# Performance work log

Measured on AMD Instinct MI355X. Metric: run time of the kernel, lower is better.

The kernel has to match this reference:

```python
import math
import jax, jax.numpy as jnp
import numpy as np

NUM_BUCKETS = 32
MAX_DISTANCE = 128
N_HEADS = 16
D_KV = 64


def relative_position_bucket(rel_pos, num_buckets=NUM_BUCKETS, max_distance=MAX_DISTANCE):
    # bidirectional=True path of the original
    n = -rel_pos
    nb = num_buckets // 2
    ret = (n < 0).astype(jnp.int32) * nb
    n = jnp.abs(n)
    max_exact = nb // 2
    is_small = n < max_exact
    val_large = max_exact + (
        jnp.log(n.astype(jnp.float32) / max_exact)
        / math.log(max_distance / max_exact)
        * (nb - max_exact)
    ).astype(jnp.int32)
    val_large = jnp.minimum(val_large, nb - 1)
    return jnp.where(is_small, n, val_large) + ret


def setup_inputs() -> dict:
    key = jax.random.key(0)
    ks = jax.random.split(key, 6)
    B, S, D = 2, 2048, 1024
    inner = N_HEADS * D_KV  # 1024
    sc = 1.0 / math.sqrt(D)
    return {
        "x": jax.random.normal(ks[0], (B, S, D), dtype=jnp.float32),
        "Wq": jax.random.normal(ks[1], (D, inner), dtype=jnp.float32) * sc,
        "Wk": jax.random.normal(ks[2], (D, inner), dtype=jnp.float32) * sc,
        "Wv": jax.random.normal(ks[3], (D, inner), dtype=jnp.float32) * sc,
        "Wo": jax.random.normal(ks[4], (inner, D), dtype=jnp.float32) * sc,
        "rel_table": jax.random.normal(ks[5], (NUM_BUCKETS, N_HEADS), dtype=jnp.float32),
        "attention_mask": jnp.zeros((B, 1, 1, S), dtype=jnp.float32),
    }


def reference(x, Wq, Wk, Wv, Wo, rel_table, attention_mask):
    B, S, D = x.shape
    H, Dk = N_HEADS, D_KV

    q = (x @ Wq).reshape(B, S, H, Dk).transpose(0, 2, 1, 3)  # bhqd
    k = (x @ Wk).reshape(B, S, H, Dk).transpose(0, 2, 1, 3)
    v = (x @ Wv).reshape(B, S, H, Dk).transpose(0, 2, 1, 3)

    # NOTE: T5 attention has no 1/sqrt(d) scaling
    scores = jnp.einsum('bhqd,bhkd->bhqk', q.astype(jnp.float32), k.astype(jnp.float32))

    pos = jnp.arange(S)
    rel_pos = pos[None, :] - pos[:, None]  # [S,S] = k_pos - q_pos
    buckets = relative_position_bucket(rel_pos)
    position_bias = jnp.transpose(rel_table[buckets], (2, 0, 1))  # [H,S,S]

    scores = scores + position_bias[None, ...] + attention_mask
    weights = jax.nn.softmax(scores, axis=-1)
    out = jnp.einsum('bhqk,bhkd->bhqd', weights, v.astype(jnp.float32))
    out = out.transpose(0, 2, 1, 3).reshape(B, S, H * Dk).astype(x.dtype)
    out = out @ Wo
    return (out, position_bias)
```

## Files before the change

kernel.cpp:

```cpp
#include <hip/hip_runtime.h>
#include <hip/hip_bf16.h>
#include <math.h>
#include <stdint.h>

typedef __bf16 bf16_t;
typedef __attribute__((ext_vector_type(8))) __bf16 bf16x8;
typedef __attribute__((ext_vector_type(4))) float f32x4;
typedef float f32x4a __attribute__((ext_vector_type(4), aligned(4)));
typedef unsigned short u16;
typedef unsigned int u32;

#define DEV static __device__ __forceinline__
#define LOG2E 1.4426950408889634f

DEV u16 f2b(float f){ bf16_t h = (bf16_t)f; return __builtin_bit_cast(u16, h); }
DEV float b2f(u16 u){ bf16_t h = __builtin_bit_cast(bf16_t, u); return (float)h; }
DEV f32x4 mfma16(bf16x8 a, bf16x8 b, f32x4 c){
  return __builtin_amdgcn_mfma_f32_16x16x32_bf16(a, b, c, 0, 0, 0);
}

#if __has_builtin(__builtin_amdgcn_exp2f)
DEV float fexp2(float x){ return __builtin_amdgcn_exp2f(x); }
#else
DEV float fexp2(float x){ return exp2f(x); }
#endif

DEV void gld16(const void* g, void* l){
  __builtin_amdgcn_global_load_lds((const __attribute__((address_space(1))) u32*)g,
                                   (__attribute__((address_space(3))) u32*)l, 16, 0, 0);
}

DEV bf16x8 ldsA64(const u16* arr, int row, int ch){
  return *(const bf16x8*)&arr[row*64 + ((ch ^ (row&7))*8)];
}
DEV bf16x8 ldsA32(const u16* arr, int row, int ch){
  return *(const bf16x8*)&arr[row*32 + ((ch ^ ((row>>1)&3))*8)];
}

__global__ __launch_bounds__(256) void k_prep(const float* __restrict__ x,
                                              const float* __restrict__ Wq, const float* __restrict__ Wk,
                                              const float* __restrict__ Wv, const float* __restrict__ Wo,
                                              const float* __restrict__ rel_table, const float* __restrict__ mask,
                                              u16* __restrict__ xh, u16* __restrict__ xl,
                                              u16* __restrict__ wth, u16* __restrict__ wot,
                                              float* __restrict__ bt, float* __restrict__ bt2,
                                              float* __restrict__ msk2){
  __shared__ float tile[64][65];
  int bid = blockIdx.x;
  int t = threadIdx.x;
  if(bid < 4096){
    size_t i = ((size_t)bid*256 + t)*4;
    float4 v = *(const float4*)(x + i);
    ushort4 hv, lv; float f, hf;
    f=v.x; hv.x=f2b(f); hf=b2f(hv.x); lv.x=f2b(f-hf);
    f=v.y; hv.y=f2b(f); hf=b2f(hv.y); lv.y=f2b(f-hf);
    f=v.z; hv.z=f2b(f); hf=b2f(hv.z); lv.z=f2b(f-hf);
    f=v.w; hv.w=f2b(f); hf=b2f(hv.w); lv.w=f2b(f-hf);
    *(ushort4*)(xh+i) = hv;
    *(ushort4*)(xl+i) = lv;
  } else if(bid < 5120){
    int rr = bid - 4096;
    int z = rr >> 8, ky = (rr >> 4) & 15, nx = rr & 15;
    const float* W = (z==0)?Wq:((z==1)?Wk:((z==2)?Wv:Wo));
    int n0 = nx*64, k0 = ky*64;
    int r = t>>6, c = t&63;
    #pragma unroll
    for(int i=0;i<16;i++){
      int row = i*4 + r;
      tile[row][c] = W[(size_t)(k0+row)*1024 + n0 + c];
    }
    __syncthreads();
    #pragma unroll
    for(int i=0;i<16;i++){
      int nrow = i*4 + r;
      float v = tile[c][nrow];
      size_t o = (size_t)(n0+nrow)*1024 + k0 + c;
      if(z<3) wth[(size_t)z*1048576 + o] = f2b(v);
      else    wot[o] = f2b(v);
    }
  } else {
    int gid = (bid-5120)*256 + t;
    if(gid < 4096) msk2[gid] = mask[gid]*LOG2E;
    int h = gid >> 12, idx = gid & 4095;
    float v = 0.f;
    if(idx < 4095){
      int delta = idx - 2047;
      int n = -delta;
      int ret = 0;
      if(n < 0){ ret = 16; n = -n; }
      int bucket;
      if(n < 8) bucket = n + ret;
      else {
        float a = (float)log((double)n * 0.125);
        float rr2 = (float)((double)a / (double)2.7725887298583984f);
        int vl = 8 + (int)(rr2 * 8.0f);
        vl = vl > 15 ? 15 : vl;
        bucket = vl + ret;
      }
      v = rel_table[bucket*16 + h];
    }
    bt[gid] = v;
    bt2[gid] = v*LOG2E - 32.0f;
  }
}

__global__ __launch_bounds__(256) void k_gemm_qkv(const u16* __restrict__ xh, const u16* __restrict__ xl,
                                                  const u16* __restrict__ wth,
                                                  u16* __restrict__ qh, u16* __restrict__ ql,
                                                  u16* __restrict__ kh, u16* __restrict__ vt){
  __shared__ __align__(16) u16 SM[17408];
  u16* Ah = SM; u16* Al = SM+4096; u16* Bh = SM+8192;
  int z = blockIdx.z;
  const u16* WH = wth + (size_t)z*1048576;
  int m0 = blockIdx.y*128, n0 = blockIdx.x*128;
  int t = threadIdx.x, w = t>>6, lane = t&63, l16 = lane&15, g = lane>>4;
  f32x4 acc[4][4];
  #pragma unroll
  for(int i=0;i<4;i++)
    #pragma unroll
    for(int j=0;j<4;j++) acc[i][j] = {0.f,0.f,0.f,0.f};
  int rbase = (w>>1)*64, cbase = (w&1)*64;
  for(int k0=0;k0<1024;k0+=32){
    __syncthreads();
    #pragma unroll
    for(int jj=0;jj<6;jj++){
      int q = w + 4*jj;
      int arr = q>>3, sub = q&7;
      if(z!=0 && arr==1) continue;
      int row = sub*16 + (lane>>2);
      int lch = (lane&3) ^ ((row>>1)&3);
      const u16* src;
      if(arr==0)      src = xh + (size_t)(m0+row)*1024 + k0 + lch*8;
      else if(arr==1) src = xl + (size_t)(m0+row)*1024 + k0 + lch*8;
      else            src = WH + (size_t)(n0+row)*1024 + k0 + lch*8;
      gld16(src, &SM[q*512]);
    }
    __syncthreads();
    if(z!=0){
      bf16x8 ah[4];
      #pragma unroll
      for(int i=0;i<4;i++) ah[i] = ldsA32(Ah, rbase + i*16 + l16, g);
      #pragma unroll
      for(int j=0;j<4;j++){
        bf16x8 bh = ldsA32(Bh, cbase + j*16 + l16, g);
        #pragma unroll
        for(int i=0;i<4;i++)
          acc[i][j] = mfma16(ah[i], bh, acc[i][j]);
      }
    } else {
      bf16x8 ah[4], am[4];
      #pragma unroll
      for(int i=0;i<4;i++){
        int row = rbase + i*16 + l16;
        ah[i] = ldsA32(Ah, row, g);
        am[i] = ldsA32(Al, row, g);
      }
      #pragma unroll
      for(int j=0;j<4;j++){
        bf16x8 bh = ldsA32(Bh, cbase + j*16 + l16, g);
        #pragma unroll
        for(int i=0;i<4;i++){
          acc[i][j] = mfma16(ah[i], bh, acc[i][j]);
          acc[i][j] = mfma16(am[i], bh, acc[i][j]);
        }
      }
    }
  }
  if(z==2){
    __syncthreads();
    #pragma unroll
    for(int i=0;i<4;i++)
      #pragma unroll
      for(int j=0;j<4;j++)
        #pragma unroll
        for(int r=0;r<4;r++){
          int ml = rbase + i*16 + g*4 + r;
          int nl = cbase + j*16 + l16;
          SM[nl*136 + ml] = f2b(acc[i][j][r]);
        }
    __syncthreads();
    int bb = m0 >> 11;
    #pragma unroll
    for(int kk=0;kk<8;kk++){
      int id = t + 256*kk;
      int row = id>>4, ch = id&15;
      uint4 v = *(const uint4*)&SM[row*136 + ch*8];
      int n = n0 + row;
      size_t dst = ((size_t)(bb*16 + (n>>6))*64 + (n&63))*2048 + (m0&2047) + ch*8;
      *(uint4*)&vt[dst] = v;
    }
  } else {
    #pragma unroll
    for(int i=0;i<4;i++)
      #pragma unroll
      for(int j=0;j<4;j++)
        #pragma unroll
        for(int r=0;r<4;r++){
          int m = m0 + rbase + i*16 + g*4 + r;
          int n = n0 + cbase + j*16 + l16;
          float v = acc[i][j][r];
          if(z==0) v *= LOG2E;
          int b = m >> 11, s = m & 2047;
          int hh = n >> 6, d = n & 63;
          size_t a = ((size_t)(b*16+hh)*2048 + s)*64 + d;
          u16 hb = f2b(v);
          if(z==0){ qh[a]=hb; ql[a]=f2b(v - b2f(hb)); }
          else    { kh[a]=hb; }
        }
  }
}

__global__ __launch_bounds__(256) void k_attn(const u16* __restrict__ qh, const u16* __restrict__ ql,
                                              const u16* __restrict__ kh,
                                              const u16* __restrict__ vt, const float* __restrict__ bt2,
                                              const float* __restrict__ msk2,
                                              const float* __restrict__ bt, float* __restrict__ bias_out,
                                              u16* __restrict__ ao){
  __shared__ __align__(16) u16 SM[12800];
  u16* KH = SM; u16* VT = SM+4096;
  int bh = blockIdx.y, b = bh>>4, h = bh&15;
  int q0 = blockIdx.x*64;
  int t = threadIdx.x, w = t>>6, lane = t&63, l16 = lane&15, g = lane>>4;
  size_t base  = (size_t)bh*2048*64;
  size_t vbase = (size_t)bh*64*2048;
  u16* PSw = SM + 8192 + w*1152;
  const float* bt2h = bt2 + h*4096;
  const float* msk2b = msk2 + b*2048;
  size_t wbase = ((size_t)(bh*32 + blockIdx.x))*65536 + t*8;

  bf16x8 qfh[2], qfl[2];
  {
    int qr = q0 + w*16 + l16;
    size_t a0 = base + (size_t)qr*64 + g*8;
    qfh[0] = *(const bf16x8*)&qh[a0];
    qfl[0] = *(const bf16x8*)&ql[a0];
    qfh[1] = *(const bf16x8*)&qh[a0+32];
    qfl[1] = *(const bf16x8*)&ql[a0+32];
  }
  f32x4 O[4];
  float rs[4];
  #pragma unroll
  for(int jd=0;jd<4;jd++) O[jd] = {0.f,0.f,0.f,0.f};
  #pragma unroll
  for(int r=0;r<4;r++) rs[r] = 0.f;
  int qgbase = q0 + w*16 + g*4;

  for(int k0=0;k0<2048;k0+=64){
    __syncthreads();
    #pragma unroll
    for(int jj=0;jj<4;jj++){
      int q = w + 4*jj;
      int arr = q>>3, sub = q&7;
      int row = sub*8 + (lane>>3);
      int lch = (lane&7) ^ (row&7);
      const u16* src;
      if(arr==0) src = kh + base + (size_t)(k0+row)*64 + lch*8;
      else       src = vt + vbase + (size_t)row*2048 + k0 + lch*8;
      gld16(src, &SM[q*512]);
    }
    {
      size_t f = wbase + (size_t)(k0>>6)*2048;
      int hh = (int)(f >> 22);
      int rem = (int)(f & 4194303);
      int qq = rem >> 11;
      int kk = rem & 2047;
      const float* row = bt + hh*4096 + (kk - qq + 2047);
      f32x4a v0 = *(const f32x4a*)(row);
      f32x4a v1 = *(const f32x4a*)(row + 4);
      *(f32x4a*)(bias_out + f)     = v0;
      *(f32x4a*)(bias_out + f + 4) = v1;
    }
    f32x4 sc[4];
    {
      const float* bb = bt2h + (k0 + l16 + 2047 - qgbase);
      #pragma unroll
      for(int j=0;j<4;j++){
        f32x4a ld = *(const f32x4a*)(bb + j*16 - 3);
        float mk = msk2b[k0 + j*16 + l16];
        sc[j] = (f32x4){ld[3]+mk, ld[2]+mk, ld[1]+mk, ld[0]+mk};
      }
    }
    __syncthreads();
    #pragma unroll
    for(int j=0;j<4;j++){
      int krow = j*16 + l16;
      bf16x8 kfh0 = ldsA64(KH, krow, g);
      bf16x8 kfh1 = ldsA64(KH, krow, 4+g);
      f32x4 s = sc[j];
      s = mfma16(qfh[0], kfh0, s);
      s = mfma16(qfl[0], kfh0, s);
      s = mfma16(qfh[1], kfh1, s);
      s = mfma16(qfl[1], kfh1, s);
      sc[j] = s;
    }
    #pragma unroll
    for(int j=0;j<4;j++){
      #pragma unroll
      for(int r=0;r<4;r++){
        float p = fexp2(sc[j][r]);
        rs[r] += p;
        PSw[(g*4+r)*72 + j*16 + l16] = f2b(p);
      }
    }
    #pragma unroll
    for(int ds=0; ds<2; ds++){
      bf16x8 pa = *(const bf16x8*)&PSw[l16*72 + ds*32 + g*8];
      #pragma unroll
      for(int jd=0;jd<4;jd++){
        bf16x8 vb = ldsA64(VT, jd*16 + l16, ds*4 + g);
        O[jd] = mfma16(pa, vb, O[jd]);
      }
    }
  }
  #pragma unroll
  for(int r=0;r<4;r++){
    float v = rs[r];
    v += __shfl_xor(v,1,64);
    v += __shfl_xor(v,2,64);
    v += __shfl_xor(v,4,64);
    v += __shfl_xor(v,8,64);
    float inv = 1.f/v;
    int q = qgbase + r;
    size_t a = ((size_t)(b*2048 + q))*1024 + h*64;
    #pragma unroll
    for(int jd=0;jd<4;jd++)
      ao[a + jd*16 + l16] = f2b(O[jd][r]*inv);
  }
}

__global__ __launch_bounds__(256) void k_gemm_out(const u16* __restrict__ ao, const u16* __restrict__ wot,
                                                  float* __restrict__ out){
  __shared__ __align__(16) u16 SM[8192];
  u16* As = SM; u16* Bs = SM+4096;
  int m0 = blockIdx.y*128, n0 = blockIdx.x*128;
  int t = threadIdx.x, w = t>>6, lane = t&63, l16 = lane&15, g = lane>>4;
  f32x4 acc[4][4];
  #pragma unroll
  for(int i=0;i<4;i++)
    #pragma unroll
    for(int j=0;j<4;j++) acc[i][j] = {0.f,0.f,0.f,0.f};
  int rbase = (w>>1)*64, cbase = (w&1)*64;
  for(int k0=0;k0<1024;k0+=32){
    __syncthreads();
    #pragma unroll
    for(int jj=0;jj<4;jj++){
      int q = w + 4*jj;
      int arr = q>>3, sub = q&7;
      int row = sub*16 + (lane>>2);
      int lch = (lane&3) ^ ((row>>1)&3);
      const u16* src;
      if(arr==0) src = ao  + (size_t)(m0+row)*1024 + k0 + lch*8;
      else       src = wot + (size_t)(n0+row)*1024 + k0 + lch*8;
      gld16(src, &SM[q*512]);
    }
    __syncthreads();
    bf16x8 af[4];
    #pragma unroll
    for(int i=0;i<4;i++) af[i] = ldsA32(As, rbase + i*16 + l16, g);
    #pragma unroll
    for(int j=0;j<4;j++){
      bf16x8 bfb = ldsA32(Bs, cbase + j*16 + l16, g);
      #pragma unroll
      for(int i=0;i<4;i++)
        acc[i][j] = mfma16(af[i], bfb, acc[i][j]);
    }
  }
  #pragma unroll
  for(int i=0;i<4;i++)
    #pragma unroll
    for(int j=0;j<4;j++)
      #pragma unroll
      for(int r=0;r<4;r++){
        int m = m0 + rbase + i*16 + g*4 + r;
        int n = n0 + cbase + j*16 + l16;
        out[(size_t)m*1024 + n] = acc[i][j][r];
      }
}

extern "C" void kernel_launch(void* const* d_in, const int* in_sizes, int n_in,
                              void* d_out, int out_size, void* d_ws, size_t ws_size,
                              hipStream_t stream) {
  const float* x   = (const float*)d_in[0];
  const float* Wq  = (const float*)d_in[1];
  const float* Wk  = (const float*)d_in[2];
  const float* Wv  = (const float*)d_in[3];
  const float* Wo  = (const float*)d_in[4];
  const float* rel = (const float*)d_in[5];
  const float* msk = (const float*)d_in[6];
  float* out = (float*)d_out;
  float* bias_out = out + (size_t)4194304;
  char* ws = (char*)d_ws;
  u16* xh  = (u16*)(ws + 0);
  u16* xl  = (u16*)(ws + 8388608);
  u16* wth = (u16*)(ws + 16777216);
  u16* wot = (u16*)(ws + 23068672);
  u16* qh  = (u16*)(ws + 25165824);
  u16* ql  = (u16*)(ws + 33554432);
  u16* kh  = (u16*)(ws + 41943040);
  u16* vt  = (u16*)(ws + 50331648);
  u16* ao  = (u16*)(ws + 58720256);
  float* bt  = (float*)(ws + 67108864);
  float* bt2 = (float*)(ws + 67371008);
  float* msk2= (float*)(ws + 67633152);

  k_prep      <<<5376, 256, 0, stream>>>(x, Wq, Wk, Wv, Wo, rel, msk,
                                         xh, xl, wth, wot, bt, bt2, msk2);
  k_gemm_qkv  <<<dim3(8,32,3), 256, 0, stream>>>(xh, xl, wth, qh, ql, kh, vt);
  k_attn      <<<dim3(32,32), 256, 0, stream>>>(qh, ql, kh, vt, bt2, msk2, bt, bias_out, ao);
  k_gemm_out  <<<dim3(8,32), 256, 0, stream>>>(ao, wot, out);
}
```

Before: 487.1 us.

## Remap block order for XCD locality, prefetch bias rows, use nontemporal stores

Both GEMM kernels and the attention kernel remap the linear block index so that consecutive blocks placed on the same XCD (round-robin by 8) work on neighbouring tiles and share L2 data. The attention kernel loads the position-bias row one iteration ahead, writes the large bias output with nontemporal stores, and adds a launch-bounds occupancy hint of 4. The output GEMM also uses nontemporal stores. The remap assumes specific grid dimensions (8 wide for the GEMMs, 32x32 for attention), and the occupancy hint can force register spilling.

```diff
diff --git a/kernel.cpp b/kernel.cpp
--- a/kernel.cpp
+++ b/kernel.cpp
@@ -112,7 +112,9 @@
   u16* Ah = SM; u16* Al = SM+4096; u16* Bh = SM+8192;
   int z = blockIdx.z;
   const u16* WH = wth + (size_t)z*1048576;
-  int m0 = blockIdx.y*128, n0 = blockIdx.x*128;
+  int lin2 = blockIdx.x + 8*blockIdx.y;
+  int nl2 = (lin2 & 7)*32 + (lin2 >> 3);
+  int n0 = (nl2 & 7)*128, m0 = (nl2 >> 3)*128;
   int t = threadIdx.x, w = t>>6, lane = t&63, l16 = lane&15, g = lane>>4;
   f32x4 acc[4][4];
   #pragma unroll
@@ -210,7 +212,7 @@
   }
 }
 
-__global__ __launch_bounds__(256) void k_attn(const u16* __restrict__ qh, const u16* __restrict__ ql,
+__global__ __launch_bounds__(256,4) void k_attn(const u16* __restrict__ qh, const u16* __restrict__ ql,
                                               const u16* __restrict__ kh,
                                               const u16* __restrict__ vt, const float* __restrict__ bt2,
                                               const float* __restrict__ msk2,
@@ -218,15 +220,18 @@
                                               u16* __restrict__ ao){
   __shared__ __align__(16) u16 SM[12800];
   u16* KH = SM; u16* VT = SM+4096;
-  int bh = blockIdx.y, b = bh>>4, h = bh&15;
-  int q0 = blockIdx.x*64;
+  int lin = blockIdx.x + 32*blockIdx.y;
+  int nlw = (lin & 7)*128 + (lin >> 3);
+  int qx = nlw & 31, bh = nlw >> 5;
+  int b = bh>>4, h = bh&15;
+  int q0 = qx*64;
   int t = threadIdx.x, w = t>>6, lane = t&63, l16 = lane&15, g = lane>>4;
   size_t base  = (size_t)bh*2048*64;
   size_t vbase = (size_t)bh*64*2048;
   u16* PSw = SM + 8192 + w*1152;
   const float* bt2h = bt2 + h*4096;
   const float* msk2b = msk2 + b*2048;
-  size_t wbase = ((size_t)(bh*32 + blockIdx.x))*65536 + t*8;
+  size_t wbase = ((size_t)(bh*32 + qx))*65536 + t*8;
 
   bf16x8 qfh[2], qfl[2];
   {
@@ -244,6 +249,18 @@
   #pragma unroll
   for(int r=0;r<4;r++) rs[r] = 0.f;
   int qgbase = q0 + w*16 + g*4;
+
+  f32x4a bv0, bv1;
+  {
+    size_t f = wbase;
+    int hh = (int)(f >> 22);
+    int rem = (int)(f & 4194303);
+    int qq = rem >> 11;
+    int kk = rem & 2047;
+    const float* row = bt + hh*4096 + (kk - qq + 2047);
+    bv0 = *(const f32x4a*)(row);
+    bv1 = *(const f32x4a*)(row + 4);
+  }
 
   for(int k0=0;k0<2048;k0+=64){
     __syncthreads();
@@ -260,15 +277,18 @@
     }
     {
       size_t f = wbase + (size_t)(k0>>6)*2048;
-      int hh = (int)(f >> 22);
-      int rem = (int)(f & 4194303);
-      int qq = rem >> 11;
-      int kk = rem & 2047;
-      const float* row = bt + hh*4096 + (kk - qq + 2047);
-      f32x4a v0 = *(const f32x4a*)(row);
-      f32x4a v1 = *(const f32x4a*)(row + 4);
-      *(f32x4a*)(bias_out + f)     = v0;
-      *(f32x4a*)(bias_out + f + 4) = v1;
+      __builtin_nontemporal_store(bv0, (f32x4a*)(bias_out + f));
+      __builtin_nontemporal_store(bv1, (f32x4a*)(bias_out + f + 4));
+      if(k0 < 2048-64){
+        size_t fn = f + 2048;
+        int hh = (int)(fn >> 22);
+        int rem = (int)(fn & 4194303);
+        int qq = rem >> 11;
+        int kk = rem & 2047;
+        const float* row = bt + hh*4096 + (kk - qq + 2047);
+        bv0 = *(const f32x4a*)(row);
+        bv1 = *(const f32x4a*)(row + 4);
+      }
     }
     f32x4 sc[4];
     {
@@ -332,7 +352,9 @@
                                                   float* __restrict__ out){
   __shared__ __align__(16) u16 SM[8192];
   u16* As = SM; u16* Bs = SM+4096;
-  int m0 = blockIdx.y*128, n0 = blockIdx.x*128;
+  int lin2 = blockIdx.x + 8*blockIdx.y;
+  int nl2 = (lin2 & 7)*32 + (lin2 >> 3);
+  int n0 = (nl2 & 7)*128, m0 = (nl2 >> 3)*128;
   int t = threadIdx.x, w = t>>6, lane = t&63, l16 = lane&15, g = lane>>4;
   f32x4 acc[4][4];
   #pragma unroll
@@ -373,7 +395,7 @@
       for(int r=0;r<4;r++){
         int m = m0 + rbase + i*16 + g*4 + r;
         int n = n0 + cbase + j*16 + l16;
-        out[(size_t)m*1024 + n] = acc[i][j][r];
+        __builtin_nontemporal_store(acc[i][j][r], &out[(size_t)m*1024 + n]);
       }
 }
 
```

Result: faster. 451.5 us (-7.3%).
